# Kernel optimization log

Measured on AMD Instinct MI355X. Metric: run time of the kernel, lower is better.

## Reference

```python
import jax, jax.numpy as jnp
import numpy as np

B, S, D = 4, 2048, 768
H = 12
HD = D // H  # 64

def setup_inputs() -> dict:
    key = jax.random.key(0)
    ks = jax.random.split(key, 5)
    scale = 0.02
    return {
        "x": jax.random.normal(ks[0], (B, S, D), dtype=jnp.float32),
        "w_qkv": jax.random.normal(ks[1], (D, 3 * D), dtype=jnp.float32) * scale,
        "b_qkv": jax.random.normal(ks[2], (3 * D,), dtype=jnp.float32) * scale,
        "w_proj": jax.random.normal(ks[3], (D, D), dtype=jnp.float32) * scale,
        "b_proj": jax.random.normal(ks[4], (D,), dtype=jnp.float32) * scale,
    }

def reference(x, w_qkv, b_qkv, w_proj, b_proj):
    bsz, seq_len, dim = x.shape
    qkv = x @ w_qkv + b_qkv                      # [B,S,3D]
    q, k, v = jnp.split(qkv, 3, axis=-1)
    # [B,S,D] -> [B,H,S,HD]
    def heads(t):
        return t.reshape(bsz, seq_len, H, HD).transpose(0, 2, 1, 3)
    q, k, v = heads(q), heads(k), heads(v)
    scores = jnp.einsum('bhqd,bhkd->bhqk', q, k) * (1.0 / np.sqrt(HD))
    causal = jnp.tril(jnp.ones((seq_len, seq_len), dtype=bool))
    scores = jnp.where(causal[None, None], scores, -jnp.inf)
    attn = jax.nn.softmax(scores.astype(jnp.float32), axis=-1).astype(scores.dtype)
    y = jnp.einsum('bhqk,bhkd->bhqd', attn, v)   # [B,H,S,HD]
    y = y.transpose(0, 2, 1, 3).reshape(bsz, seq_len, dim)
    return y @ w_proj + b_proj
```

## Files before the change

kernel.cpp:

```cpp
#include <hip/hip_runtime.h>
#include <hip/hip_bf16.h>
#include <cstdint>

#define BDIM 768
#define HN 12
#define HDIM 64
#define SEQ 2048
#define BATCH 4
#define MTOT (BATCH * SEQ)

typedef __attribute__((ext_vector_type(8))) short bfrag;
typedef __attribute__((ext_vector_type(4))) float f32x4;

union pfu { bfrag f; unsigned u[4]; };

static __device__ __forceinline__ unsigned short f2bf(float f) {
    union { float f; unsigned u; } v; v.f = f;
    unsigned r = v.u + 0x7FFF + ((v.u >> 16) & 1);
    return (unsigned short)(r >> 16);
}

static __device__ __forceinline__ float fexp2(float x) {
    float r; asm("v_exp_f32 %0, %1" : "=v"(r) : "v"(x)); return r;
}

static __device__ __forceinline__ unsigned cvt_pk_bf16(float lo, float hi) {
    unsigned r;
    asm("v_cvt_pk_bf16_f32 %0, %1, %2" : "=v"(r) : "v"(lo), "v"(hi));
    return r;
}

#if __has_builtin(__builtin_amdgcn_permlane32_swap) && __has_builtin(__builtin_amdgcn_permlane16_swap)
#define HAVE_PERMLANE 1
#else
#define HAVE_PERMLANE 0
#endif

static __device__ __forceinline__ float redmax16(float x) {
#if HAVE_PERMLANE
    union { float f; unsigned u; } a; a.f = x;
    auto r = __builtin_amdgcn_permlane16_swap(a.u, a.u, false, false);
    union { unsigned u; float f; } p, q; p.u = r[0]; q.u = r[1];
    return fmaxf(p.f, q.f);
#else
    return fmaxf(x, __shfl_xor(x, 16));
#endif
}

static __device__ __forceinline__ float redmax32(float x) {
#if HAVE_PERMLANE
    union { float f; unsigned u; } a; a.f = x;
    auto r = __builtin_amdgcn_permlane32_swap(a.u, a.u, false, false);
    union { unsigned u; float f; } p, q; p.u = r[0]; q.u = r[1];
    return fmaxf(p.f, q.f);
#else
    return fmaxf(x, __shfl_xor(x, 32));
#endif
}

static __device__ void transpose_tile(
    const float* __restrict__ in, unsigned short* __restrict__ out,
    int R, int C, int cb, int rb, unsigned short (*t)[72])
{
    const int tid = threadIdx.x;
    const int c0 = cb * 64, r0 = rb * 64;
    #pragma unroll
    for (int i = 0; i < 4; ++i) {
        const int r = (tid >> 4) + i * 16;
        const int c = (tid & 15) * 4;
        const float4 v = *(const float4*)&in[(size_t)(r0 + r) * C + c0 + c];
        t[c + 0][r] = f2bf(v.x);
        t[c + 1][r] = f2bf(v.y);
        t[c + 2][r] = f2bf(v.z);
        t[c + 3][r] = f2bf(v.w);
    }
    __syncthreads();
    #pragma unroll
    for (int i = 0; i < 2; ++i) {
        const int c = (tid >> 3) + i * 32;
        const int r = (tid & 7) * 8;
        *(bfrag*)&out[(size_t)(c0 + c) * R + r0 + r] = *(const bfrag*)&t[c][r];
    }
}

__global__ __launch_bounds__(256) void prep_all(
    const float* __restrict__ x, unsigned short* __restrict__ xb,
    const float* __restrict__ w_qkv, unsigned short* __restrict__ wqT,
    const float* __restrict__ w_proj, unsigned short* __restrict__ wpT,
    int* __restrict__ qctr)
{
    __shared__ unsigned short t[64][72];
    const int bid = blockIdx.x;
    if (bid == 0 && threadIdx.x < 8) qctr[threadIdx.x] = 0;

    if (bid < 3072) {
        const int i = bid * 256 + threadIdx.x;
        const float4 a = ((const float4*)x)[i * 2];
        const float4 b = ((const float4*)x)[i * 2 + 1];
        bfrag o;
        o[0] = f2bf(a.x); o[1] = f2bf(a.y); o[2] = f2bf(a.z); o[3] = f2bf(a.w);
        o[4] = f2bf(b.x); o[5] = f2bf(b.y); o[6] = f2bf(b.z); o[7] = f2bf(b.w);
        ((bfrag*)xb)[i] = o;
    } else if (bid < 3504) {
        const int idx = bid - 3072;
        transpose_tile(w_qkv, wqT, BDIM, 3 * BDIM, idx % 36, idx / 36, t);
    } else {
        const int idx = bid - 3504;
        transpose_tile(w_proj, wpT, BDIM, BDIM, idx % 12, idx / 12, t);
    }
}

#define VT_STRIDE 136

__global__ __launch_bounds__(256) void gemm_qkv(
    const unsigned short* __restrict__ A,
    const unsigned short* __restrict__ Bt,
    const float* __restrict__ bias,
    unsigned short* __restrict__ qb,
    unsigned short* __restrict__ kb,
    unsigned short* __restrict__ vTt)
{
    __shared__ unsigned short Sh[128 * VT_STRIDE];
    unsigned short* As = Sh;
    unsigned short* Bs = Sh + 128 * 64;

    const int tid  = threadIdx.x;
    const int lane = tid & 63;
    const int wid  = tid >> 6;
    const int l15  = lane & 15;
    const int l4   = lane >> 4;

    const int nwg  = (int)(gridDim.x * gridDim.y);
    const int flat = (int)(blockIdx.y * gridDim.x + blockIdx.x);
    const int swz  = (flat & 7) * (nwg >> 3) + (flat >> 3);
    const int m0 = (swz / (int)gridDim.x) * 128;
    const int n0 = (swz % (int)gridDim.x) * 128;

    const int wm = (wid >> 1) * 64;
    const int wn = (wid & 1) * 64;

    f32x4 acc[4][4] = {};

    for (int k0 = 0; k0 < BDIM; k0 += 64) {
        __syncthreads();
        #pragma unroll
        for (int i = 0; i < 4; ++i) {
            const int row = wid * 32 + i * 8 + (lane >> 3);
            const int ck  = (((lane & 7) ^ (row & 7)) * 8);
            __builtin_amdgcn_global_load_lds(
                (const __attribute__((address_space(1))) void*)(A + (size_t)(m0 + row) * BDIM + k0 + ck),
                (__attribute__((address_space(3))) void*)(As + (wid * 4 + i) * 512),
                16, 0, 0);
            __builtin_amdgcn_global_load_lds(
                (const __attribute__((address_space(1))) void*)(Bt + (size_t)(n0 + row) * BDIM + k0 + ck),
                (__attribute__((address_space(3))) void*)(Bs + (wid * 4 + i) * 512),
                16, 0, 0);
        }
        __syncthreads();

        #pragma unroll
        for (int ks = 0; ks < 2; ++ks) {
            bfrag af[4], bfv[4];
            #pragma unroll
            for (int mi = 0; mi < 4; ++mi) {
                const int row = wm + mi * 16 + l15;
                const int ch  = (ks * 4 + l4) ^ (row & 7);
                af[mi] = *(const bfrag*)(As + row * 64 + ch * 8);
            }
            #pragma unroll
            for (int ni = 0; ni < 4; ++ni) {
                const int row = wn + ni * 16 + l15;
                const int ch  = (ks * 4 + l4) ^ (row & 7);
                bfv[ni] = *(const bfrag*)(Bs + row * 64 + ch * 8);
            }
            #pragma unroll
            for (int mi = 0; mi < 4; ++mi)
                #pragma unroll
                for (int ni = 0; ni < 4; ++ni)
                    acc[mi][ni] = __builtin_amdgcn_mfma_f32_16x16x32_bf16(
                        af[mi], bfv[ni], acc[mi][ni], 0, 0, 0);
        }
    }

    if (n0 < 1536) {
        unsigned short* dst = (n0 < 768) ? qb : kb;
        const int coff = (n0 < 768) ? 0 : 768;
        #pragma unroll
        for (int mi = 0; mi < 4; ++mi)
            #pragma unroll
            for (int ni = 0; ni < 4; ++ni) {
                const int n = n0 + wn + ni * 16 + l15;
                const float bv = bias[n];
                #pragma unroll
                for (int r = 0; r < 4; ++r) {
                    const int m = m0 + wm + mi * 16 + l4 * 4 + r;
                    dst[(size_t)m * BDIM + (n - coff)] = f2bf(acc[mi][ni][r] + bv);
                }
            }
    } else {
        __syncthreads();
        #pragma unroll
        for (int mi = 0; mi < 4; ++mi)
            #pragma unroll
            for (int ni = 0; ni < 4; ++ni) {
                const int n = n0 + wn + ni * 16 + l15;
                const float bv = bias[n];
                const int drow = wn + ni * 16 + l15;
                #pragma unroll
                for (int r = 0; r < 4; ++r) {
                    const int mcol = wm + mi * 16 + l4 * 4 + r;
                    Sh[drow * VT_STRIDE + mcol] = f2bf(acc[mi][ni][r] + bv);
                }
            }
        __syncthreads();
        const int drow = tid >> 1;
        const int ch0  = (tid & 1) * 64;
        const size_t vrow = (size_t)(m0 >> 11) * 768 + (n0 - 1536) + drow;
        unsigned short* dp = vTt + vrow * SEQ + (m0 & (SEQ - 1)) + ch0;
        #pragma unroll
        for (int i = 0; i < 8; ++i)
            *(bfrag*)(dp + i * 8) = *(const bfrag*)(Sh + drow * VT_STRIDE + ch0 + i * 8);
    }
}

__global__ __launch_bounds__(256) void gemm_proj(
    const unsigned short* __restrict__ A,
    const unsigned short* __restrict__ Bt,
    const float* __restrict__ bias,
    float* __restrict__ C)
{
    __shared__ unsigned short As[64 * 64];
    __shared__ unsigned short Bs[128 * 64];

    const int tid  = threadIdx.x;
    const int lane = tid & 63;
    const int wid  = tid >> 6;
    const int l15  = lane & 15;
    const int l4   = lane >> 4;

    const int nwg  = (int)(gridDim.x * gridDim.y);
    const int flat = (int)(blockIdx.y * gridDim.x + blockIdx.x);
    const int swz  = (flat & 7) * (nwg >> 3) + (flat >> 3);
    const int m0 = (swz / (int)gridDim.x) * 64;
    const int n0 = (swz % (int)gridDim.x) * 128;

    const int wm = (wid >> 1) * 32;
    const int wn = (wid & 1) * 64;

    f32x4 acc[2][4] = {};

    for (int k0 = 0; k0 < BDIM; k0 += 64) {
        __syncthreads();
        #pragma unroll
        for (int i = 0; i < 2; ++i) {
            const int row = wid * 16 + i * 8 + (lane >> 3);
            const int ck  = (((lane & 7) ^ (row & 7)) * 8);
            __builtin_amdgcn_global_load_lds(
                (const __attribute__((address_space(1))) void*)(A + (size_t)(m0 + row) * BDIM + k0 + ck),
                (__attribute__((address_space(3))) void*)(As + (wid * 16 + i * 8) * 64),
                16, 0, 0);
        }
        #pragma unroll
        for (int i = 0; i < 4; ++i) {
            const int row = wid * 32 + i * 8 + (lane >> 3);
            const int ck  = (((lane & 7) ^ (row & 7)) * 8);
            __builtin_amdgcn_global_load_lds(
                (const __attribute__((address_space(1))) void*)(Bt + (size_t)(n0 + row) * BDIM + k0 + ck),
                (__attribute__((address_space(3))) void*)(Bs + (wid * 32 + i * 8) * 64),
                16, 0, 0);
        }
        __syncthreads();

        #pragma unroll
        for (int ks = 0; ks < 2; ++ks) {
            bfrag af[2], bfv[4];
            #pragma unroll
            for (int mi = 0; mi < 2; ++mi) {
                const int row = wm + mi * 16 + l15;
                const int ch  = (ks * 4 + l4) ^ (row & 7);
                af[mi] = *(const bfrag*)(As + row * 64 + ch * 8);
            }
            #pragma unroll
            for (int ni = 0; ni < 4; ++ni) {
                const int row = wn + ni * 16 + l15;
                const int ch  = (ks * 4 + l4) ^ (row & 7);
                bfv[ni] = *(const bfrag*)(Bs + row * 64 + ch * 8);
            }
            #pragma unroll
            for (int mi = 0; mi < 2; ++mi)
                #pragma unroll
                for (int ni = 0; ni < 4; ++ni)
                    acc[mi][ni] = __builtin_amdgcn_mfma_f32_16x16x32_bf16(
                        af[mi], bfv[ni], acc[mi][ni], 0, 0, 0);
        }
    }

    #pragma unroll
    for (int mi = 0; mi < 2; ++mi)
        #pragma unroll
        for (int ni = 0; ni < 4; ++ni) {
            const int n = n0 + wn + ni * 16 + l15;
            const float bv = bias[n];
            #pragma unroll
            for (int r = 0; r < 4; ++r) {
                const int m = m0 + wm + mi * 16 + l4 * 4 + r;
                C[(size_t)m * BDIM + n] = acc[mi][ni][r] + bv;
            }
        }
}

#define C2 0.18033688011112042f
#define THR 8.0f

__global__ __launch_bounds__(256, 2) void attn_flash_mfma(
    const unsigned short* __restrict__ qb,
    const unsigned short* __restrict__ kb,
    const unsigned short* __restrict__ vT,
    unsigned short* __restrict__ yatt,
    int* __restrict__ qctr)
{
    __shared__ unsigned short Ks[2][64 * 64];
    __shared__ unsigned short Vs[2][64 * 64];

    const int hint = blockIdx.x & 7;
    const int tid  = threadIdx.x;
    const int lane = tid & 63;
    const int wid  = tid >> 6;
    const int l15  = lane & 15;
    const int l4   = lane >> 4;

    bfrag onesf;
    #pragma unroll
    for (int j = 0; j < 8; ++j) onesf[j] = (short)0x3F80;

    for (;;) {
        __syncthreads();
        if (tid == 0) *(int*)&Ks[0][0] = atomicAdd(&qctr[hint], 1);
        __syncthreads();
        const int it = *(const int*)&Ks[0][0];
        if (it >= 96) break;
        __syncthreads();

        const int bh = hint * 6 + (it % 6);
        const int p  = 15 - (it / 6);
        const int h = bh % HN, b = bh / HN;
        const int q0 = p * 128;
        const int ktmax = 2 * p + 1;

        const unsigned short* kg = kb + (size_t)b * SEQ * BDIM + h * HDIM;
        const unsigned short* vg = vT + (size_t)bh * HDIM * SEQ;

        bfrag qf[2][2];
        {
            const unsigned short* qr0 =
                qb + (size_t)(b * SEQ + q0 + wid * 16 + l15) * BDIM + h * HDIM;
            qf[0][0] = *(const bfrag*)(qr0 + l4 * 8);
            qf[0][1] = *(const bfrag*)(qr0 + 32 + l4 * 8);
            const unsigned short* qr1 = qr0 + (size_t)64 * BDIM;
            qf[1][0] = *(const bfrag*)(qr1 + l4 * 8);
            qf[1][1] = *(const bfrag*)(qr1 + 32 + l4 * 8);
        }

        f32x4 acc0[4] = {}, acc1[4] = {};
        f32x4 accl0 = {}, accl1 = {};
        float m0v = -3.0e38f, m1v = -3.0e38f;

        pfu pf0[2], pf1[2];
        bfrag vr[2][4];
        #pragma unroll
        for (int ks = 0; ks < 2; ++ks) {
            #pragma unroll
            for (int i = 0; i < 4; ++i) { pf0[ks].u[i] = 0u; pf1[ks].u[i] = 0u; }
            #pragma unroll
            for (int ds = 0; ds < 4; ++ds)
                #pragma unroll
                for (int j = 0; j < 8; ++j) vr[ks][ds][j] = 0;
        }

        auto stage = [&](int bufi, int ktile) {
            const int k0 = ktile * 64;
            #pragma unroll
            for (int i = 0; i < 2; ++i) {
                const int row = wid * 16 + i * 8 + (lane >> 3);
                const int ck  = ((lane & 7) ^ (row & 7)) * 8;
                __builtin_amdgcn_global_load_lds(
                    (const __attribute__((address_space(1))) void*)(kg + (size_t)(k0 + row) * BDIM + ck),
                    (__attribute__((address_space(3))) void*)(&Ks[bufi][(wid * 16 + i * 8) * 64]),
                    16, 0, 0);
                __builtin_amdgcn_global_load_lds(
                    (const __attribute__((address_space(1))) void*)(vg + (size_t)row * SEQ + k0 + ck),
                    (__attribute__((address_space(3))) void*)(&Vs[bufi][(wid * 16 + i * 8) * 64]),
                    16, 0, 0);
            }
        };

        auto softmax_dance = [&](f32x4* s, float& mm, pfu* pf, f32x4* acc, f32x4& accl) {
            float t0 = fmaxf(s[0][0], s[0][1]);
            float t1 = fmaxf(s[0][2], s[0][3]);
            float t2 = fmaxf(s[1][0], s[1][1]);
            float t3 = fmaxf(s[1][2], s[1][3]);
            float t4 = fmaxf(s[2][0], s[2][1]);
            float t5 = fmaxf(s[2][2], s[2][3]);
            float t6 = fmaxf(s[3][0], s[3][1]);
            float t7 = fmaxf(s[3][2], s[3][3]);
            t0 = fmaxf(t0, t1); t2 = fmaxf(t2, t3);
            t4 = fmaxf(t4, t5); t6 = fmaxf(t6, t7);
            t0 = fmaxf(t0, t2); t4 = fmaxf(t4, t6);
            float mx = fmaxf(t0, t4);
            mx = redmax16(mx);
            mx = redmax32(mx);
            const float mx2 = mx * C2;

            if (!__all(mx2 <= mm + THR)) {
                const float mnew = fmaxf(mm, mx2);
                const float fac  = fexp2(mm - mnew);
                mm = mnew;
                #pragma unroll
                for (int r = 0; r < 4; ++r) {
                    const float fr = __shfl(fac, (lane & 48) | (l4 * 4 + r));
                    #pragma unroll
                    for (int ds = 0; ds < 4; ++ds) acc[ds][r] *= fr;
                    accl[r] *= fr;
                }
            }

            #pragma unroll
            for (int cs = 0; cs < 4; ++cs)
                #pragma unroll
                for (int r = 0; r < 4; ++r)
                    s[cs][r] = fexp2(fmaf(s[cs][r], C2, -mm));

            unsigned pk[4][2];
            #pragma unroll
            for (int cs = 0; cs < 4; ++cs) {
                pk[cs][0] = cvt_pk_bf16(s[cs][0], s[cs][1]);
                pk[cs][1] = cvt_pk_bf16(s[cs][2], s[cs][3]);
            }
            #pragma unroll
            for (int ks = 0; ks < 2; ++ks)
                #pragma unroll
                for (int i = 0; i < 2; ++i) {
#if HAVE_PERMLANE
                    auto r1 = __builtin_amdgcn_permlane32_swap(
                        pk[ks * 2][i], pk[ks * 2 + 1][i], false, false);
                    auto r2 = __builtin_amdgcn_permlane16_swap(r1[0], r1[1], false, false);
                    pf[ks].u[i]     = r2[0];
                    pf[ks].u[2 + i] = r2[1];
#else
                    const unsigned A  = pk[ks * 2][i];
                    const unsigned B  = pk[ks * 2 + 1][i];
                    const unsigned Ax = __shfl_xor(A, 32);
                    const unsigned Bx = __shfl_xor(B, 32);
                    const unsigned P1 = (l4 < 2) ? A : Bx;
                    const unsigned P2 = (l4 < 2) ? Ax : B;
                    const unsigned S1 = __shfl_xor(P1, 16);
                    const unsigned S2 = __shfl_xor(P2, 16);
                    pf[ks].u[i]     = (l4 & 1) ? S2 : P1;
                    pf[ks].u[2 + i] = (l4 & 1) ? P2 : S1;
#endif
                }
        };

        stage(0, 0);
        __syncthreads();

        int buf = 0;
        for (int kt = 0;;) {
            if (kt < ktmax) stage(buf ^ 1, kt + 1);

            const unsigned short* Kb = Ks[buf];
            const unsigned short* Vb = Vs[buf];

            f32x4 s0[4] = {}, s1[4] = {};
            __builtin_amdgcn_s_setprio(1);
            #pragma unroll
            for (int ks = 0; ks < 2; ++ks) {
                #pragma unroll
                for (int cs = 0; cs < 4; ++cs) {
                    const int row = cs * 16 + l15;
                    const int ch  = (ks * 4 + l4) ^ (row & 7);
                    const bfrag kf = *(const bfrag*)(Kb + row * 64 + ch * 8);
                    s0[cs] = __builtin_amdgcn_mfma_f32_16x16x32_bf16(kf, qf[0][ks], s0[cs], 0, 0, 0);
                    s1[cs] = __builtin_amdgcn_mfma_f32_16x16x32_bf16(kf, qf[1][ks], s1[cs], 0, 0, 0);
                }
            }
            #pragma unroll
            for (int ks = 0; ks < 2; ++ks) {
                #pragma unroll
                for (int ds = 0; ds < 4; ++ds) {
                    acc0[ds] = __builtin_amdgcn_mfma_f32_16x16x32_bf16(pf0[ks].f, vr[ks][ds], acc0[ds], 0, 0, 0);
                    acc1[ds] = __builtin_amdgcn_mfma_f32_16x16x32_bf16(pf1[ks].f, vr[ks][ds], acc1[ds], 0, 0, 0);
                }
                accl0 = __builtin_amdgcn_mfma_f32_16x16x32_bf16(pf0[ks].f, onesf, accl0, 0, 0, 0);
                accl1 = __builtin_amdgcn_mfma_f32_16x16x32_bf16(pf1[ks].f, onesf, accl1, 0, 0, 0);
            }
            __builtin_amdgcn_s_setprio(0);

            #pragma unroll
            for (int ks = 0; ks < 2; ++ks)
                #pragma unroll
                for (int ds = 0; ds < 4; ++ds) {
                    const int vrow = ds * 16 + l15;
                    const int vch  = (ks * 4 + l4) ^ (vrow & 7);
                    vr[ks][ds] = *(const bfrag*)(Vb + vrow * 64 + vch * 8);
                }

            if (kt >= 2 * p) {
                const int qg = q0 + wid * 16 + l15;
                #pragma unroll
                for (int cs = 0; cs < 4; ++cs)
                    #pragma unroll
                    for (int r = 0; r < 4; ++r) {
                        const int kgl = kt * 64 + cs * 16 + l4 * 4 + r;
                        if (kgl > qg)      s0[cs][r] = -3.0e38f;
                        if (kgl > qg + 64) s1[cs][r] = -3.0e38f;
                    }
            }

            softmax_dance(s0, m0v, pf0, acc0, accl0);
            softmax_dance(s1, m1v, pf1, acc1, accl1);

            if (kt == ktmax) break;
            __syncthreads();
            buf ^= 1; ++kt;
        }

        #pragma unroll
        for (int ks = 0; ks < 2; ++ks) {
            #pragma unroll
            for (int ds = 0; ds < 4; ++ds) {
                acc0[ds] = __builtin_amdgcn_mfma_f32_16x16x32_bf16(pf0[ks].f, vr[ks][ds], acc0[ds], 0, 0, 0);
                acc1[ds] = __builtin_amdgcn_mfma_f32_16x16x32_bf16(pf1[ks].f, vr[ks][ds], acc1[ds], 0, 0, 0);
            }
            accl0 = __builtin_amdgcn_mfma_f32_16x16x32_bf16(pf0[ks].f, onesf, accl0, 0, 0, 0);
            accl1 = __builtin_amdgcn_mfma_f32_16x16x32_bf16(pf1[ks].f, onesf, accl1, 0, 0, 0);
        }

        #pragma unroll
        for (int r = 0; r < 4; ++r) {
            const float iv0 = 1.f / accl0[r];
            const float iv1 = 1.f / accl1[r];
            unsigned short* o0 =
                yatt + (size_t)(b * SEQ + q0 + wid * 16 + l4 * 4 + r) * BDIM + h * HDIM;
            unsigned short* o1 = o0 + (size_t)64 * BDIM;
            #pragma unroll
            for (int ds = 0; ds < 4; ++ds) {
                o0[ds * 16 + l15] = f2bf(acc0[ds][r] * iv0);
                o1[ds * 16 + l15] = f2bf(acc1[ds][r] * iv1);
            }
        }
    }
}

extern "C" void kernel_launch(void* const* d_in, const int* in_sizes, int n_in,
                              void* d_out, int out_size, void* d_ws, size_t ws_size,
                              hipStream_t stream)
{
    const float* x      = (const float*)d_in[0];
    const float* w_qkv  = (const float*)d_in[1];
    const float* b_qkv  = (const float*)d_in[2];
    const float* w_proj = (const float*)d_in[3];
    const float* b_proj = (const float*)d_in[4];
    float* out = (float*)d_out;

    unsigned short* xb   = (unsigned short*)d_ws;
    unsigned short* qb   = xb  + (size_t)MTOT * BDIM;
    unsigned short* kbuf = qb  + (size_t)MTOT * BDIM;
    unsigned short* vT   = kbuf + (size_t)MTOT * BDIM;
    unsigned short* yatt = vT  + (size_t)MTOT * BDIM;
    unsigned short* wqT  = yatt + (size_t)MTOT * BDIM;
    unsigned short* wpT  = wqT + (size_t)3 * BDIM * BDIM;
    int*            qctr = (int*)(wpT + (size_t)BDIM * BDIM);

    prep_all<<<dim3(3648), 256, 0, stream>>>(
        x, xb, w_qkv, wqT, w_proj, wpT, qctr);

    gemm_qkv<<<dim3(3 * BDIM / 128, MTOT / 128), 256, 0, stream>>>(
        xb, wqT, b_qkv, qb, kbuf, vT);

    attn_flash_mfma<<<dim3(640), 256, 0, stream>>>(qb, kbuf, vT, yatt, qctr);

    gemm_proj<<<dim3(BDIM / 128, MTOT / 64), 256, 0, stream>>>(
        yatt, wpT, b_proj, out);
}
```

Before: 135.0 us.

## Replace atomic work queue with static paired causal tiles of 64 query rows

The attention kernel drops its persistent atomic-counter scheduler, which took 128-row query tiles in descending order. It now launches a fixed grid of 768 blocks, and each block handles two 64-row query tiles (j and 31-j) so that causal work is balanced statically. Each wave keeps one 16-row Q fragment instead of two, which lowers register pressure and removes the counter reset from the prep kernel. In exchange, every K/V tile is loaded once per 64 query rows instead of once per 128, which roughly doubles K/V staging traffic and the number of barriers.

```diff
diff --git a/kernel.cpp b/kernel.cpp
--- a/kernel.cpp
+++ b/kernel.cpp
@@ -86,12 +86,10 @@
 __global__ __launch_bounds__(256) void prep_all(
     const float* __restrict__ x, unsigned short* __restrict__ xb,
     const float* __restrict__ w_qkv, unsigned short* __restrict__ wqT,
-    const float* __restrict__ w_proj, unsigned short* __restrict__ wpT,
-    int* __restrict__ qctr)
+    const float* __restrict__ w_proj, unsigned short* __restrict__ wpT)
 {
     __shared__ unsigned short t[64][72];
     const int bid = blockIdx.x;
-    if (bid == 0 && threadIdx.x < 8) qctr[threadIdx.x] = 0;
 
     if (bid < 3072) {
         const int i = bid * 256 + threadIdx.x;
@@ -316,13 +314,18 @@
     const unsigned short* __restrict__ qb,
     const unsigned short* __restrict__ kb,
     const unsigned short* __restrict__ vT,
-    unsigned short* __restrict__ yatt,
-    int* __restrict__ qctr)
+    unsigned short* __restrict__ yatt)
 {
     __shared__ unsigned short Ks[2][64 * 64];
     __shared__ unsigned short Vs[2][64 * 64];
 
-    const int hint = blockIdx.x & 7;
+    const int bid  = blockIdx.x;
+    const int hint = bid & 7;
+    const int idx  = bid >> 3;
+    const int bh   = hint * 6 + idx % 6;
+    const int jj   = idx / 6;
+    const int h = bh % HN, b = bh / HN;
+
     const int tid  = threadIdx.x;
     const int lane = tid & 63;
     const int wid  = tid >> 6;
@@ -333,68 +336,54 @@
     #pragma unroll
     for (int j = 0; j < 8; ++j) onesf[j] = (short)0x3F80;
 
-    for (;;) {
-        __syncthreads();
-        if (tid == 0) *(int*)&Ks[0][0] = atomicAdd(&qctr[hint], 1);
-        __syncthreads();
-        const int it = *(const int*)&Ks[0][0];
-        if (it >= 96) break;
-        __syncthreads();
-
-        const int bh = hint * 6 + (it % 6);
-        const int p  = 15 - (it / 6);
-        const int h = bh % HN, b = bh / HN;
-        const int q0 = p * 128;
-        const int ktmax = 2 * p + 1;
-
-        const unsigned short* kg = kb + (size_t)b * SEQ * BDIM + h * HDIM;
-        const unsigned short* vg = vT + (size_t)bh * HDIM * SEQ;
-
-        bfrag qf[2][2];
-        {
-            const unsigned short* qr0 =
-                qb + (size_t)(b * SEQ + q0 + wid * 16 + l15) * BDIM + h * HDIM;
-            qf[0][0] = *(const bfrag*)(qr0 + l4 * 8);
-            qf[0][1] = *(const bfrag*)(qr0 + 32 + l4 * 8);
-            const unsigned short* qr1 = qr0 + (size_t)64 * BDIM;
-            qf[1][0] = *(const bfrag*)(qr1 + l4 * 8);
-            qf[1][1] = *(const bfrag*)(qr1 + 32 + l4 * 8);
-        }
-
-        f32x4 acc0[4] = {}, acc1[4] = {};
-        f32x4 accl0 = {}, accl1 = {};
-        float m0v = -3.0e38f, m1v = -3.0e38f;
-
-        pfu pf0[2], pf1[2];
+    const unsigned short* kg = kb + (size_t)b * SEQ * BDIM + h * HDIM;
+    const unsigned short* vg = vT + (size_t)bh * HDIM * SEQ;
+
+    auto stage = [&](int bufi, int ktile) {
+        const int k0 = ktile * 64;
+        #pragma unroll
+        for (int i = 0; i < 2; ++i) {
+            const int row = wid * 16 + i * 8 + (lane >> 3);
+            const int ck  = ((lane & 7) ^ (row & 7)) * 8;
+            __builtin_amdgcn_global_load_lds(
+                (const __attribute__((address_space(1))) void*)(kg + (size_t)(k0 + row) * BDIM + ck),
+                (__attribute__((address_space(3))) void*)(&Ks[bufi][(wid * 16 + i * 8) * 64]),
+                16, 0, 0);
+            __builtin_amdgcn_global_load_lds(
+                (const __attribute__((address_space(1))) void*)(vg + (size_t)row * SEQ + k0 + ck),
+                (__attribute__((address_space(3))) void*)(&Vs[bufi][(wid * 16 + i * 8) * 64]),
+                16, 0, 0);
+        }
+    };
+
+    #pragma unroll 1
+    for (int seg = 0; seg < 2; ++seg) {
+        const int qt = seg ? (31 - jj) : jj;
+        const int q0 = qt * 64;
+        const int ktmax = qt;
+
+        const unsigned short* qr0 =
+            qb + (size_t)(b * SEQ + q0 + wid * 16 + l15) * BDIM + h * HDIM;
+        const bfrag qf0 = *(const bfrag*)(qr0 + l4 * 8);
+        const bfrag qf1 = *(const bfrag*)(qr0 + 32 + l4 * 8);
+
+        f32x4 acc[4] = {};
+        f32x4 accl   = {};
+        float m = -3.0e38f;
+
+        pfu pf[2];
         bfrag vr[2][4];
         #pragma unroll
         for (int ks = 0; ks < 2; ++ks) {
             #pragma unroll
-            for (int i = 0; i < 4; ++i) { pf0[ks].u[i] = 0u; pf1[ks].u[i] = 0u; }
+            for (int i = 0; i < 4; ++i) pf[ks].u[i] = 0u;
             #pragma unroll
             for (int ds = 0; ds < 4; ++ds)
                 #pragma unroll
                 for (int j = 0; j < 8; ++j) vr[ks][ds][j] = 0;
         }
 
-        auto stage = [&](int bufi, int ktile) {
-            const int k0 = ktile * 64;
-            #pragma unroll
-            for (int i = 0; i < 2; ++i) {
-                const int row = wid * 16 + i * 8 + (lane >> 3);
-                const int ck  = ((lane & 7) ^ (row & 7)) * 8;
-                __builtin_amdgcn_global_load_lds(
-                    (const __attribute__((address_space(1))) void*)(kg + (size_t)(k0 + row) * BDIM + ck),
-                    (__attribute__((address_space(3))) void*)(&Ks[bufi][(wid * 16 + i * 8) * 64]),
-                    16, 0, 0);
-                __builtin_amdgcn_global_load_lds(
-                    (const __attribute__((address_space(1))) void*)(vg + (size_t)row * SEQ + k0 + ck),
-                    (__attribute__((address_space(3))) void*)(&Vs[bufi][(wid * 16 + i * 8) * 64]),
-                    16, 0, 0);
-            }
-        };
-
-        auto softmax_dance = [&](f32x4* s, float& mm, pfu* pf, f32x4* acc, f32x4& accl) {
+        auto softmax_dance = [&](f32x4* s) {
             float t0 = fmaxf(s[0][0], s[0][1]);
             float t1 = fmaxf(s[0][2], s[0][3]);
             float t2 = fmaxf(s[1][0], s[1][1]);
@@ -411,10 +400,10 @@
             mx = redmax32(mx);
             const float mx2 = mx * C2;
 
-            if (!__all(mx2 <= mm + THR)) {
-                const float mnew = fmaxf(mm, mx2);
-                const float fac  = fexp2(mm - mnew);
-                mm = mnew;
+            if (!__all(mx2 <= m + THR)) {
+                const float mnew = fmaxf(m, mx2);
+                const float fac  = fexp2(m - mnew);
+                m = mnew;
                 #pragma unroll
                 for (int r = 0; r < 4; ++r) {
                     const float fr = __shfl(fac, (lane & 48) | (l4 * 4 + r));
@@ -428,7 +417,7 @@
             for (int cs = 0; cs < 4; ++cs)
                 #pragma unroll
                 for (int r = 0; r < 4; ++r)
-                    s[cs][r] = fexp2(fmaf(s[cs][r], C2, -mm));
+                    s[cs][r] = fexp2(fmaf(s[cs][r], C2, -m));
 
             unsigned pk[4][2];
             #pragma unroll
@@ -461,6 +450,7 @@
                 }
         };
 
+        __syncthreads();
         stage(0, 0);
         __syncthreads();
 
@@ -471,28 +461,26 @@
             const unsigned short* Kb = Ks[buf];
             const unsigned short* Vb = Vs[buf];
 
-            f32x4 s0[4] = {}, s1[4] = {};
+            f32x4 s[4] = {};
             __builtin_amdgcn_s_setprio(1);
             #pragma unroll
             for (int ks = 0; ks < 2; ++ks) {
+                const bfrag qk = ks ? qf1 : qf0;
                 #pragma unroll
                 for (int cs = 0; cs < 4; ++cs) {
                     const int row = cs * 16 + l15;
                     const int ch  = (ks * 4 + l4) ^ (row & 7);
                     const bfrag kf = *(const bfrag*)(Kb + row * 64 + ch * 8);
-                    s0[cs] = __builtin_amdgcn_mfma_f32_16x16x32_bf16(kf, qf[0][ks], s0[cs], 0, 0, 0);
-                    s1[cs] = __builtin_amdgcn_mfma_f32_16x16x32_bf16(kf, qf[1][ks], s1[cs], 0, 0, 0);
+                    s[cs] = __builtin_amdgcn_mfma_f32_16x16x32_bf16(kf, qk, s[cs], 0, 0, 0);
                 }
             }
             #pragma unroll
             for (int ks = 0; ks < 2; ++ks) {
                 #pragma unroll
-                for (int ds = 0; ds < 4; ++ds) {
-                    acc0[ds] = __builtin_amdgcn_mfma_f32_16x16x32_bf16(pf0[ks].f, vr[ks][ds], acc0[ds], 0, 0, 0);
-                    acc1[ds] = __builtin_amdgcn_mfma_f32_16x16x32_bf16(pf1[ks].f, vr[ks][ds], acc1[ds], 0, 0, 0);
-                }
-                accl0 = __builtin_amdgcn_mfma_f32_16x16x32_bf16(pf0[ks].f, onesf, accl0, 0, 0, 0);
-                accl1 = __builtin_amdgcn_mfma_f32_16x16x32_bf16(pf1[ks].f, onesf, accl1, 0, 0, 0);
+                for (int ds = 0; ds < 4; ++ds)
+                    acc[ds] = __builtin_amdgcn_mfma_f32_16x16x32_bf16(
+                        pf[ks].f, vr[ks][ds], acc[ds], 0, 0, 0);
+                accl = __builtin_amdgcn_mfma_f32_16x16x32_bf16(pf[ks].f, onesf, accl, 0, 0, 0);
             }
             __builtin_amdgcn_s_setprio(0);
 
@@ -505,20 +493,16 @@
                     vr[ks][ds] = *(const bfrag*)(Vb + vrow * 64 + vch * 8);
                 }
 
-            if (kt >= 2 * p) {
-                const int qg = q0 + wid * 16 + l15;
+            if (kt == ktmax) {
                 #pragma unroll
                 for (int cs = 0; cs < 4; ++cs)
                     #pragma unroll
-                    for (int r = 0; r < 4; ++r) {
-                        const int kgl = kt * 64 + cs * 16 + l4 * 4 + r;
-                        if (kgl > qg)      s0[cs][r] = -3.0e38f;
-                        if (kgl > qg + 64) s1[cs][r] = -3.0e38f;
-                    }
-            }
-
-            softmax_dance(s0, m0v, pf0, acc0, accl0);
-            softmax_dance(s1, m1v, pf1, acc1, accl1);
+                    for (int r = 0; r < 4; ++r)
+                        if (cs * 16 + l4 * 4 + r > wid * 16 + l15)
+                            s[cs][r] = -3.0e38f;
+            }
+
+            softmax_dance(s);
 
             if (kt == ktmax) break;
             __syncthreads();
@@ -528,26 +512,20 @@
         #pragma unroll
         for (int ks = 0; ks < 2; ++ks) {
             #pragma unroll
-            for (int ds = 0; ds < 4; ++ds) {
-                acc0[ds] = __builtin_amdgcn_mfma_f32_16x16x32_bf16(pf0[ks].f, vr[ks][ds], acc0[ds], 0, 0, 0);
-                acc1[ds] = __builtin_amdgcn_mfma_f32_16x16x32_bf16(pf1[ks].f, vr[ks][ds], acc1[ds], 0, 0, 0);
-            }
-            accl0 = __builtin_amdgcn_mfma_f32_16x16x32_bf16(pf0[ks].f, onesf, accl0, 0, 0, 0);
-            accl1 = __builtin_amdgcn_mfma_f32_16x16x32_bf16(pf1[ks].f, onesf, accl1, 0, 0, 0);
+            for (int ds = 0; ds < 4; ++ds)
+                acc[ds] = __builtin_amdgcn_mfma_f32_16x16x32_bf16(
+                    pf[ks].f, vr[ks][ds], acc[ds], 0, 0, 0);
+            accl = __builtin_amdgcn_mfma_f32_16x16x32_bf16(pf[ks].f, onesf, accl, 0, 0, 0);
         }
 
         #pragma unroll
         for (int r = 0; r < 4; ++r) {
-            const float iv0 = 1.f / accl0[r];
-            const float iv1 = 1.f / accl1[r];
-            unsigned short* o0 =
+            const float iv = 1.f / accl[r];
+            unsigned short* o =
                 yatt + (size_t)(b * SEQ + q0 + wid * 16 + l4 * 4 + r) * BDIM + h * HDIM;
-            unsigned short* o1 = o0 + (size_t)64 * BDIM;
-            #pragma unroll
-            for (int ds = 0; ds < 4; ++ds) {
-                o0[ds * 16 + l15] = f2bf(acc0[ds][r] * iv0);
-                o1[ds * 16 + l15] = f2bf(acc1[ds][r] * iv1);
-            }
+            #pragma unroll
+            for (int ds = 0; ds < 4; ++ds)
+                o[ds * 16 + l15] = f2bf(acc[ds][r] * iv);
         }
     }
 }
@@ -570,15 +548,14 @@
     unsigned short* yatt = vT  + (size_t)MTOT * BDIM;
     unsigned short* wqT  = yatt + (size_t)MTOT * BDIM;
     unsigned short* wpT  = wqT + (size_t)3 * BDIM * BDIM;
-    int*            qctr = (int*)(wpT + (size_t)BDIM * BDIM);
 
     prep_all<<<dim3(3648), 256, 0, stream>>>(
-        x, xb, w_qkv, wqT, w_proj, wpT, qctr);
+        x, xb, w_qkv, wqT, w_proj, wpT);
 
     gemm_qkv<<<dim3(3 * BDIM / 128, MTOT / 128), 256, 0, stream>>>(
         xb, wqT, b_qkv, qb, kbuf, vT);
 
-    attn_flash_mfma<<<dim3(640), 256, 0, stream>>>(qb, kbuf, vT, yatt, qctr);
+    attn_flash_mfma<<<dim3(768), 256, 0, stream>>>(qb, kbuf, vT, yatt);
 
     gemm_proj<<<dim3(BDIM / 128, MTOT / 64), 256, 0, stream>>>(
         yatt, wpT, b_proj, out);
```

Measured after the change: 125.4 us. 1.08x faster.
